# Performance work log

Hardware: AMD Instinct MI355X
Metric: run time of the kernel (lower is better)

## Reference

```python
import jax, jax.numpy as jnp
import numpy as np

B, N, F, H = 4, 512, 64, 128
EPS = 0.0            # GINE eps (train_eps=False)
NEG_SLOPE = 0.01     # leaky_relu negative slope


def setup_inputs() -> dict:
    key = jax.random.key(0)
    ks = jax.random.split(key, 8)
    x = jax.random.normal(ks[0], (B, N, F), dtype=jnp.float32)
    adj = jax.random.uniform(ks[1], (B, N, N), dtype=jnp.float32)
    edge_attr = jax.random.normal(ks[2], (B, N, N, F), dtype=jnp.float32)
    mask = jax.random.randint(ks[3], (B, N), 0, 2) > 0  # bool (B,N)
    W1 = jax.random.normal(ks[4], (F, H), dtype=jnp.float32) / np.sqrt(F)
    b1 = jnp.zeros((H,), dtype=jnp.float32)
    W2 = jax.random.normal(ks[5], (H, F), dtype=jnp.float32) / np.sqrt(H)
    b2 = jnp.zeros((F,), dtype=jnp.float32)
    return {"x": x, "adj": adj, "edge_attr": edge_attr, "mask": mask,
            "W1": W1, "b1": b1, "W2": W2, "b2": b2}


def reference(x, adj, edge_attr, mask, W1, b1, W2, b2):
    # z[b,i,j,f] = x[b,i,f] + edge_attr[b,i,j,f]
    # msg = leaky_relu(adj[b,i,j] * z); aggregate over source axis i (dim 1)
    msg = jax.nn.leaky_relu(adj[..., None] * (x[:, :, None, :] + edge_attr),
                            negative_slope=NEG_SLOPE)
    agg = jnp.sum(msg, axis=1)                      # (B, N, F), indexed by j
    out = (1.0 + EPS) * x + agg                     # add_loop=True
    # nn applied on masked rows, zeros elsewhere (equivalent to out[mask]=nn(out[mask]))
    h = jax.nn.leaky_relu(out @ W1 + b1, negative_slope=NEG_SLOPE) @ W2 + b2
    return jnp.where(mask[..., None], h, jnp.zeros((), dtype=h.dtype))
```

## Files before the change

### kernel.cpp

```cpp
#include <hip/hip_runtime.h>


namespace {

constexpr int Bc = 4;
constexpr int Nc = 512;
constexpr int Fc = 64;
constexpr int Hc = 128;
constexpr int TJ = 4;
constexpr int TH = 512;
constexpr float NEG = 0.01f;

__device__ __forceinline__ float lrelu(float z) {
  return z > 0.f ? z : z * NEG;
}

__global__ __launch_bounds__(TH, 4) void gine_fused(
    const float* __restrict__ x,
    const float* __restrict__ adj,
    const float* __restrict__ ea,
    const int* __restrict__ mask,
    const float* __restrict__ W1,
    const float* __restrict__ b1,
    const float* __restrict__ W2,
    const float* __restrict__ b2,
    float* __restrict__ out)
{
  const int blk = blockIdx.x;
  const int b   = blk >> 7;
  const int j0  = (blk & 127) * TJ;
  const int tid = threadIdx.x;
  const int f4  = tid & 15;
  const int jl  = (tid >> 4) & 3;
  const int ip  = tid >> 6;

  __shared__ float4 s_adj4[Nc];
  __shared__ float4 s_part[TH];
  __shared__ float  s_out[TJ][Fc];
  __shared__ float  s_hid[TJ][Hc];

  const float* adjb = adj + (size_t)b * Nc * Nc;
  s_adj4[tid] = *reinterpret_cast<const float4*>(adjb + (size_t)tid * Nc + j0);
  __syncthreads();

  const float4* xb4 = reinterpret_cast<const float4*>(x + (size_t)b * Nc * Fc);
  const float4* eap = reinterpret_cast<const float4*>(ea)
                    + ((size_t)b * Nc * Nc + (j0 + jl)) * (Fc / 4) + f4;
  constexpr int ISTRIDE = Nc * Fc / 4;

  float4 acc = make_float4(0.f, 0.f, 0.f, 0.f);
  #pragma unroll 4
  for (int i = ip; i < Nc; i += 8) {
    const float a   = reinterpret_cast<const float*>(&s_adj4[i])[jl];
    const float4 xv = xb4[i * (Fc / 4) + f4];
    const float4 ev = eap[(size_t)i * ISTRIDE];
    acc.x += lrelu(a * (xv.x + ev.x));
    acc.y += lrelu(a * (xv.y + ev.y));
    acc.z += lrelu(a * (xv.z + ev.z));
    acc.w += lrelu(a * (xv.w + ev.w));
  }

  s_part[tid] = acc;
  __syncthreads();
  #pragma unroll
  for (int s = 256; s >= 64; s >>= 1) {
    if (tid < s) {
      float4 p = s_part[tid];
      const float4 q = s_part[tid + s];
      p.x += q.x; p.y += q.y; p.z += q.z; p.w += q.w;
      s_part[tid] = p;
    }
    __syncthreads();
  }

  if (tid < 64) {
    const int row = tid >> 4;
    const int fg  = tid & 15;
    float4 r = s_part[tid];
    const float4 xj = xb4[(j0 + row) * (Fc / 4) + fg];
    r.x += xj.x; r.y += xj.y; r.z += xj.z; r.w += xj.w;
    reinterpret_cast<float4*>(&s_out[row][0])[fg] = r;
  }
  __syncthreads();

  {
    const int row = tid >> 7;
    const int h   = tid & 127;
    float hv = b1[h];
    #pragma unroll 8
    for (int f = 0; f < Fc; ++f)
      hv = fmaf(s_out[row][f], W1[f * Hc + h], hv);
    s_hid[row][h] = lrelu(hv);
  }
  __syncthreads();

  if (tid < TJ * Fc) {
    const int row = tid >> 6;
    const int f   = tid & 63;
    float o = b2[f];
    #pragma unroll 8
    for (int h = 0; h < Hc; ++h)
      o = fmaf(s_hid[row][h], W2[h * Fc + f], o);
    const int rowg = b * Nc + j0 + row;
    out[rowg * Fc + f] = (mask[rowg] != 0) ? o : 0.f;
  }
}

}

extern "C" void kernel_launch(void* const* d_in, const int* in_sizes, int n_in,
                              void* d_out, int out_size, void* d_ws, size_t ws_size,
                              hipStream_t stream) {
  const float* x    = (const float*)d_in[0];
  const float* adj  = (const float*)d_in[1];
  const float* ea   = (const float*)d_in[2];
  const int*   mask = (const int*)d_in[3];
  const float* W1   = (const float*)d_in[4];
  const float* b1   = (const float*)d_in[5];
  const float* W2   = (const float*)d_in[6];
  const float* b2   = (const float*)d_in[7];
  float* out = (float*)d_out;

  gine_fused<<<dim3(Bc * Nc / TJ), dim3(TH), 0, stream>>>(
      x, adj, ea, mask, W1, b1, W2, b2, out);
}
```

Before: 378.8 us.

## Split aggregation into source-chunk partial sums with contiguous edge reads

```diff
diff --git a/kernel.cpp b/kernel.cpp
--- a/kernel.cpp
+++ b/kernel.cpp
@@ -7,72 +7,117 @@
 constexpr int Nc = 512;
 constexpr int Fc = 64;
 constexpr int Hc = 128;
+constexpr int CI = 8;
+constexpr int NCHUNK = Nc / CI;
 constexpr int TJ = 4;
-constexpr int TH = 512;
 constexpr float NEG = 0.01f;
 
 __device__ __forceinline__ float lrelu(float z) {
   return z > 0.f ? z : z * NEG;
 }
 
-__global__ __launch_bounds__(TH, 4) void gine_fused(
+__global__ __launch_bounds__(1024, 1) void gine_phase1(
     const float* __restrict__ x,
     const float* __restrict__ adj,
     const float* __restrict__ ea,
+    float* __restrict__ partial)
+{
+  const int blk = blockIdx.x;
+  const int b   = blk >> 6;
+  const int c   = blk & 63;
+  const int i0  = c * CI;
+  const int tid = threadIdx.x;
+
+  __shared__ float s_acc[Nc * Fc];
+  __shared__ float s_adj[CI * Nc];
+  __shared__ float s_x[CI * Fc];
+
+  float4* acc4 = reinterpret_cast<float4*>(s_acc);
+  const float4 z4 = make_float4(0.f, 0.f, 0.f, 0.f);
+  #pragma unroll
+  for (int k = 0; k < 8; ++k) acc4[tid + k * 1024] = z4;
+
+  reinterpret_cast<float4*>(s_adj)[tid] =
+      reinterpret_cast<const float4*>(adj + ((size_t)b * Nc + i0) * Nc)[tid];
+  if (tid < CI * Fc / 4)
+    reinterpret_cast<float4*>(s_x)[tid] =
+        reinterpret_cast<const float4*>(x + ((size_t)b * Nc + i0) * Fc)[tid];
+  __syncthreads();
+
+  const float4* eab = reinterpret_cast<const float4*>(ea)
+                    + ((size_t)b * Nc + i0) * Nc * (Fc / 4);
+  const float4* s_x4 = reinterpret_cast<const float4*>(s_x);
+
+  for (int r = 0; r < CI; ++r) {
+    const float4* row = eab + (size_t)r * Nc * (Fc / 4);
+    float4 ev[8];
+    #pragma unroll
+    for (int k = 0; k < 8; ++k) ev[k] = row[tid + k * 1024];
+    #pragma unroll
+    for (int k = 0; k < 8; ++k) {
+      const int q  = tid + k * 1024;
+      const int j  = q >> 4;
+      const int fg = q & 15;
+      const float a   = s_adj[r * Nc + j];
+      const float4 xv = s_x4[r * (Fc / 4) + fg];
+      float4 p = acc4[q];
+      p.x += lrelu(a * (xv.x + ev[k].x));
+      p.y += lrelu(a * (xv.y + ev[k].y));
+      p.z += lrelu(a * (xv.z + ev[k].z));
+      p.w += lrelu(a * (xv.w + ev[k].w));
+      acc4[q] = p;
+    }
+  }
+
+  float4* part = reinterpret_cast<float4*>(partial) + (size_t)blk * (Nc * Fc / 4);
+  #pragma unroll
+  for (int k = 0; k < 8; ++k) part[tid + k * 1024] = acc4[tid + k * 1024];
+}
+
+__global__ __launch_bounds__(512, 4) void gine_phase2(
+    const float* __restrict__ partial,
+    const float* __restrict__ x,
     const int* __restrict__ mask,
-    const float* __restrict__ W1,
-    const float* __restrict__ b1,
-    const float* __restrict__ W2,
-    const float* __restrict__ b2,
+    const float* __restrict__ W1, const float* __restrict__ b1,
+    const float* __restrict__ W2, const float* __restrict__ b2,
     float* __restrict__ out)
 {
   const int blk = blockIdx.x;
   const int b   = blk >> 7;
   const int j0  = (blk & 127) * TJ;
   const int tid = threadIdx.x;
-  const int f4  = tid & 15;
-  const int jl  = (tid >> 4) & 3;
-  const int ip  = tid >> 6;
+  const int lane6 = tid & 63;
+  const int f4  = lane6 & 15;
+  const int jl  = lane6 >> 4;
+  const int cp  = tid >> 6;
 
-  __shared__ float4 s_adj4[Nc];
-  __shared__ float4 s_part[TH];
+  __shared__ float4 s_part[512];
   __shared__ float  s_out[TJ][Fc];
   __shared__ float  s_hid[TJ][Hc];
 
-  const float* adjb = adj + (size_t)b * Nc * Nc;
-  s_adj4[tid] = *reinterpret_cast<const float4*>(adjb + (size_t)tid * Nc + j0);
-  __syncthreads();
-
-  const float4* xb4 = reinterpret_cast<const float4*>(x + (size_t)b * Nc * Fc);
-  const float4* eap = reinterpret_cast<const float4*>(ea)
-                    + ((size_t)b * Nc * Nc + (j0 + jl)) * (Fc / 4) + f4;
-  constexpr int ISTRIDE = Nc * Fc / 4;
-
-  float4 acc = make_float4(0.f, 0.f, 0.f, 0.f);
-  #pragma unroll 4
-  for (int i = ip; i < Nc; i += 8) {
-    const float a   = reinterpret_cast<const float*>(&s_adj4[i])[jl];
-    const float4 xv = xb4[i * (Fc / 4) + f4];
-    const float4 ev = eap[(size_t)i * ISTRIDE];
-    acc.x += lrelu(a * (xv.x + ev.x));
-    acc.y += lrelu(a * (xv.y + ev.y));
-    acc.z += lrelu(a * (xv.z + ev.z));
-    acc.w += lrelu(a * (xv.w + ev.w));
+  const float4* pb = reinterpret_cast<const float4*>(partial)
+                   + (size_t)(b * NCHUNK) * (Nc * Fc / 4)
+                   + (j0 + jl) * (Fc / 4) + f4;
+  float4 s = make_float4(0.f, 0.f, 0.f, 0.f);
+  #pragma unroll
+  for (int c = cp; c < NCHUNK; c += 8) {
+    const float4 v = pb[(size_t)c * (Nc * Fc / 4)];
+    s.x += v.x; s.y += v.y; s.z += v.z; s.w += v.w;
   }
-
-  s_part[tid] = acc;
+  s_part[tid] = s;
   __syncthreads();
   #pragma unroll
-  for (int s = 256; s >= 64; s >>= 1) {
-    if (tid < s) {
+  for (int st = 256; st >= 64; st >>= 1) {
+    if (tid < st) {
       float4 p = s_part[tid];
-      const float4 q = s_part[tid + s];
+      const float4 q = s_part[tid + st];
       p.x += q.x; p.y += q.y; p.z += q.z; p.w += q.w;
       s_part[tid] = p;
     }
     __syncthreads();
   }
 
+  const float4* xb4 = reinterpret_cast<const float4*>(x + (size_t)b * Nc * Fc);
   if (tid < 64) {
     const int row = tid >> 4;
     const int fg  = tid & 15;
@@ -120,7 +165,9 @@
   const float* W2   = (const float*)d_in[6];
   const float* b2   = (const float*)d_in[7];
   float* out = (float*)d_out;
+  float* partial = (float*)d_ws;
 
-  gine_fused<<<dim3(Bc * Nc / TJ), dim3(TH), 0, stream>>>(
-      x, adj, ea, mask, W1, b1, W2, b2, out);
+  gine_phase1<<<dim3(Bc * NCHUNK), dim3(1024), 0, stream>>>(x, adj, ea, partial);
+  gine_phase2<<<dim3(Bc * Nc / TJ), dim3(512), 0, stream>>>(
+      partial, x, mask, W1, b1, W2, b2, out);
 }
```

New measurement: 390.3 us. +3.0%, slower.
